# Kernel tuning notes

Measured on AMD Instinct MI355X. Metric: run time of the kernel, lower is better.

Reference implementation:

```python
import jax, jax.numpy as jnp
import numpy as np

BATCH, NODES, FEAT, OUT, EIG = 32, 20000, 64, 64, 16

def setup_inputs() -> dict:
    key = jax.random.key(0)
    k1, k2, k3 = jax.random.split(key, 3)
    x = jax.random.normal(k1, (BATCH, NODES, FEAT), dtype=jnp.float32)
    V = jax.random.normal(k2, (NODES, EIG), dtype=jnp.float32)
    # G packs the ParameterList: G[j, i] == self.G[j*num_features + i]
    # (full EIG x EIG matrices; xavier_uniform_ overwrites the diag init)
    G = jax.random.normal(k3, (OUT, FEAT, EIG, EIG), dtype=jnp.float32) * 0.2
    return {"x": x, "V": V, "G": G}

def reference(x, V, G):
    # original: out[b, n, j] = sum_i (V @ G[j,i] @ V.T @ x[b,:,i]) [n]
    # z[b, i, f] = sum_m V[m, f] * x[b, m, i]        (project onto eigenbasis)
    z = jnp.einsum('mf,bmi->bif', V, x)
    # w[b, j, e] = sum_{i, f} G[j, i, e, f] * z[b, i, f]  (spectral filter mix)
    w = jnp.einsum('jief,bif->bje', G, z)
    # out[b, n, j] = sum_e V[n, e] * w[b, j, e]      (back to node space)
    out = jnp.einsum('ne,bje->bnj', V, w)
    return out
```

## Files before the change

kernel.cpp:

```cpp
#include <hip/hip_runtime.h>

#define BATCH 32
#define NODES 20000
#define FEAT  64
#define OUT   64
#define EIG   16

#define CH1     32
#define S1_NPB  640
#define S1_NPW  160

__global__ void k_zero(float* __restrict__ p, int n) {
    int idx = blockIdx.x * blockDim.x + threadIdx.x;
    if (idx < n) p[idx] = 0.0f;
}

__global__ __launch_bounds__(256)
void k_stage1(const float* __restrict__ x, const float* __restrict__ V,
              float* __restrict__ z) {
    const int c = blockIdx.x;
    const int b = blockIdx.y;
    const int t = threadIdx.x;
    const int lane = t & 63;
    const int wv   = t >> 6;
    const int ms   = lane >> 4;
    const int ig   = lane & 15;

    float4 acc[4][4];
#pragma unroll
    for (int ii = 0; ii < 4; ii++)
#pragma unroll
        for (int q = 0; q < 4; q++) acc[ii][q] = make_float4(0.f,0.f,0.f,0.f);

    const int wb = c * S1_NPB + wv * S1_NPW;
    if (wb < NODES) {
        const float* xp = x + ((size_t)b * NODES + wb + ms) * FEAT + ig * 4;
        const float* vp = V + (size_t)(wb + ms) * EIG;

#pragma unroll 2
        for (int mm = 0; mm < S1_NPW / 4; mm++) {
            const float4 xv = *(const float4*)(xp + (size_t)mm * 4 * FEAT);
            const float4 v0 = *(const float4*)(vp + (size_t)mm * 4 * EIG);
            const float4 v1 = *(const float4*)(vp + (size_t)mm * 4 * EIG + 4);
            const float4 v2 = *(const float4*)(vp + (size_t)mm * 4 * EIG + 8);
            const float4 v3 = *(const float4*)(vp + (size_t)mm * 4 * EIG + 12);
            acc[0][0].x += xv.x*v0.x; acc[0][0].y += xv.x*v0.y; acc[0][0].z += xv.x*v0.z; acc[0][0].w += xv.x*v0.w;
            acc[0][1].x += xv.x*v1.x; acc[0][1].y += xv.x*v1.y; acc[0][1].z += xv.x*v1.z; acc[0][1].w += xv.x*v1.w;
            acc[0][2].x += xv.x*v2.x; acc[0][2].y += xv.x*v2.y; acc[0][2].z += xv.x*v2.z; acc[0][2].w += xv.x*v2.w;
            acc[0][3].x += xv.x*v3.x; acc[0][3].y += xv.x*v3.y; acc[0][3].z += xv.x*v3.z; acc[0][3].w += xv.x*v3.w;
            acc[1][0].x += xv.y*v0.x; acc[1][0].y += xv.y*v0.y; acc[1][0].z += xv.y*v0.z; acc[1][0].w += xv.y*v0.w;
            acc[1][1].x += xv.y*v1.x; acc[1][1].y += xv.y*v1.y; acc[1][1].z += xv.y*v1.z; acc[1][1].w += xv.y*v1.w;
            acc[1][2].x += xv.y*v2.x; acc[1][2].y += xv.y*v2.y; acc[1][2].z += xv.y*v2.z; acc[1][2].w += xv.y*v2.w;
            acc[1][3].x += xv.y*v3.x; acc[1][3].y += xv.y*v3.y; acc[1][3].z += xv.y*v3.z; acc[1][3].w += xv.y*v3.w;
            acc[2][0].x += xv.z*v0.x; acc[2][0].y += xv.z*v0.y; acc[2][0].z += xv.z*v0.z; acc[2][0].w += xv.z*v0.w;
            acc[2][1].x += xv.z*v1.x; acc[2][1].y += xv.z*v1.y; acc[2][1].z += xv.z*v1.z; acc[2][1].w += xv.z*v1.w;
            acc[2][2].x += xv.z*v2.x; acc[2][2].y += xv.z*v2.y; acc[2][2].z += xv.z*v2.z; acc[2][2].w += xv.z*v2.w;
            acc[2][3].x += xv.z*v3.x; acc[2][3].y += xv.z*v3.y; acc[2][3].z += xv.z*v3.z; acc[2][3].w += xv.z*v3.w;
            acc[3][0].x += xv.w*v0.x; acc[3][0].y += xv.w*v0.y; acc[3][0].z += xv.w*v0.z; acc[3][0].w += xv.w*v0.w;
            acc[3][1].x += xv.w*v1.x; acc[3][1].y += xv.w*v1.y; acc[3][1].z += xv.w*v1.z; acc[3][1].w += xv.w*v1.w;
            acc[3][2].x += xv.w*v2.x; acc[3][2].y += xv.w*v2.y; acc[3][2].z += xv.w*v2.z; acc[3][2].w += xv.w*v2.w;
            acc[3][3].x += xv.w*v3.x; acc[3][3].y += xv.w*v3.y; acc[3][3].z += xv.w*v3.z; acc[3][3].w += xv.w*v3.w;
        }
    }

#pragma unroll
    for (int ii = 0; ii < 4; ii++)
#pragma unroll
        for (int q = 0; q < 4; q++) {
            acc[ii][q].x += __shfl_xor(acc[ii][q].x, 16); acc[ii][q].x += __shfl_xor(acc[ii][q].x, 32);
            acc[ii][q].y += __shfl_xor(acc[ii][q].y, 16); acc[ii][q].y += __shfl_xor(acc[ii][q].y, 32);
            acc[ii][q].z += __shfl_xor(acc[ii][q].z, 16); acc[ii][q].z += __shfl_xor(acc[ii][q].z, 32);
            acc[ii][q].w += __shfl_xor(acc[ii][q].w, 16); acc[ii][q].w += __shfl_xor(acc[ii][q].w, 32);
        }

    __shared__ float4 zred[4][16][17];
    if (ms == 0) {
#pragma unroll
        for (int ii = 0; ii < 4; ii++)
#pragma unroll
            for (int q = 0; q < 4; q++) zred[wv][ig][ii * 4 + q] = acc[ii][q];
    }
    __syncthreads();

    const int i = t >> 2, q = t & 3;
    const float4 s0 = zred[0][i >> 2][(i & 3) * 4 + q];
    const float4 s1 = zred[1][i >> 2][(i & 3) * 4 + q];
    const float4 s2 = zred[2][i >> 2][(i & 3) * 4 + q];
    const float4 s3 = zred[3][i >> 2][(i & 3) * 4 + q];
    float* zp = z + (size_t)b * (FEAT * EIG) + (size_t)i * EIG + q * 4;
    atomicAdd(zp + 0, s0.x + s1.x + s2.x + s3.x);
    atomicAdd(zp + 1, s0.y + s1.y + s2.y + s3.y);
    atomicAdd(zp + 2, s0.z + s1.z + s2.z + s3.z);
    atomicAdd(zp + 3, s0.w + s1.w + s2.w + s3.w);
}

__global__ void k_stage2(const float* __restrict__ G, const float* __restrict__ z,
                         float* __restrict__ w) {
    const int j = blockIdx.x;
    const int t = threadIdx.x;
    const int e  = t & 15;
    const int bh = t >> 4;

    __shared__ float zs[32][128];
    const float* Gj = G + (size_t)j * FEAT * EIG * EIG;
    float acc0 = 0.f, acc1 = 0.f;

    for (int i0 = 0; i0 < FEAT; i0 += 8) {
        if (i0) __syncthreads();
#pragma unroll
        for (int r = 0; r < 4; r++) {
            const int g = t + 256 * r;
            const int bb = g >> 5, rem = g & 31;
            ((float4*)&zs[bb][0])[rem] =
                ((const float4*)z)[(size_t)bb * 256 + i0 * 4 + rem];
        }
        __syncthreads();

#pragma unroll 2
        for (int it = 0; it < 8; it++) {
            const int i = i0 + it;
            const float4* gp = (const float4*)(Gj + ((size_t)i * EIG + e) * EIG);
            const float4 g0 = gp[0], g1 = gp[1], g2 = gp[2], g3 = gp[3];
            const float4* zA = (const float4*)&zs[bh][it * 16];
            const float4* zB = (const float4*)&zs[bh + 16][it * 16];
            const float4 a0 = zA[0], a1 = zA[1], a2 = zA[2], a3 = zA[3];
            const float4 b0 = zB[0], b1 = zB[1], b2 = zB[2], b3 = zB[3];
            acc0 += g0.x*a0.x + g0.y*a0.y + g0.z*a0.z + g0.w*a0.w
                  + g1.x*a1.x + g1.y*a1.y + g1.z*a1.z + g1.w*a1.w
                  + g2.x*a2.x + g2.y*a2.y + g2.z*a2.z + g2.w*a2.w
                  + g3.x*a3.x + g3.y*a3.y + g3.z*a3.z + g3.w*a3.w;
            acc1 += g0.x*b0.x + g0.y*b0.y + g0.z*b0.z + g0.w*b0.w
                  + g1.x*b1.x + g1.y*b1.y + g1.z*b1.z + g1.w*b1.w
                  + g2.x*b2.x + g2.y*b2.y + g2.z*b2.z + g2.w*b2.w
                  + g3.x*b3.x + g3.y*b3.y + g3.z*b3.z + g3.w*b3.w;
        }
    }

    w[((size_t)bh * OUT + j) * EIG + e]        = acc0;
    w[((size_t)(bh+16) * OUT + j) * EIG + e]   = acc1;
}

#define DOT16(u) (v0.x*W[u][0].x + v0.y*W[u][0].y + v0.z*W[u][0].z + v0.w*W[u][0].w \
                + v1.x*W[u][1].x + v1.y*W[u][1].y + v1.z*W[u][1].z + v1.w*W[u][1].w \
                + v2.x*W[u][2].x + v2.y*W[u][2].y + v2.z*W[u][2].z + v2.w*W[u][2].w \
                + v3.x*W[u][3].x + v3.y*W[u][3].y + v3.z*W[u][3].z + v3.w*W[u][3].w)

#define CH3 64

__global__ __launch_bounds__(128)
void k_stage3(const float* __restrict__ V, const float* __restrict__ w,
              float* __restrict__ out) {
    const int c = blockIdx.x;
    const int b = blockIdx.y;
    const int t = threadIdx.x;
    const int jg = t & 15;
    const int ns = t >> 4;

    const float* wp = w + ((size_t)b * OUT + 4 * jg) * EIG;
    float4 W[4][4];
#pragma unroll
    for (int u = 0; u < 4; u++)
#pragma unroll
        for (int vr = 0; vr < 4; vr++)
            W[u][vr] = *(const float4*)(wp + u * EIG + vr * 4);

    const int nb = c * 320 + ns;
    float* ob = out + (size_t)b * NODES * OUT + 4 * jg;

#pragma unroll 2
    for (int it = 0; it < 40; it++) {
        const int n = nb + it * 8;
        if (n < NODES) {
            const float* vp = V + (size_t)n * EIG;
            const float4 v0 = *(const float4*)(vp);
            const float4 v1 = *(const float4*)(vp + 4);
            const float4 v2 = *(const float4*)(vp + 8);
            const float4 v3 = *(const float4*)(vp + 12);
            float4 o;
            o.x = DOT16(0);
            o.y = DOT16(1);
            o.z = DOT16(2);
            o.w = DOT16(3);
            *(float4*)(ob + (size_t)n * OUT) = o;
        }
    }
}

extern "C" void kernel_launch(void* const* d_in, const int* in_sizes, int n_in,
                              void* d_out, int out_size, void* d_ws, size_t ws_size,
                              hipStream_t stream) {
    const float* x = (const float*)d_in[0];
    const float* V = (const float*)d_in[1];
    const float* G = (const float*)d_in[2];
    float* out = (float*)d_out;

    float* z = (float*)d_ws;
    float* w = z + (size_t)BATCH * FEAT * EIG;

    const int zn = BATCH * FEAT * EIG;
    k_zero<<<(zn + 255) / 256, 256, 0, stream>>>(z, zn);

    k_stage1<<<dim3(CH1, BATCH), 256, 0, stream>>>(x, V, z);
    k_stage2<<<OUT, 256, 0, stream>>>(G, z, w);
    k_stage3<<<dim3(CH3, BATCH), 128, 0, stream>>>(V, w, out);
}
```

Before: 353.4 us.

## Double-buffer stage1 via LDS async loads, deterministic partial reduction, split stage2, prefetch stage3

Stage1 now streams x and V tiles into LDS with global_load_lds double buffering and writes per-chunk partial sums instead of atomics. A new reduce kernel sums the partials and zeroes w. Stage2 splits the feature loop across 8 blocks per output and accumulates into w with atomics. Stage3 software-prefetches the next V row and sets an occupancy hint. Together these aim to hide load latency and raise parallelism in the small stages, at the cost of an extra launch and partial-buffer traffic.

New measurement: 323.6 us. 1.09x faster.

```diff
diff --git a/kernel.cpp b/kernel.cpp
--- a/kernel.cpp
+++ b/kernel.cpp
@@ -1,4 +1,5 @@
 #include <hip/hip_runtime.h>
+#include <stdint.h>
 
 #define BATCH 32
 #define NODES 20000
@@ -6,18 +7,27 @@
 #define OUT   64
 #define EIG   16
 
-#define CH1     32
-#define S1_NPB  640
-#define S1_NPW  160
-
-__global__ void k_zero(float* __restrict__ p, int n) {
-    int idx = blockIdx.x * blockDim.x + threadIdx.x;
-    if (idx < n) p[idx] = 0.0f;
-}
+#define CH1      25
+#define S1_NPB   800
+#define S1_TILES 10
+#define S1_TR    80
+
+__device__ __forceinline__ void g2l16(const float* g, float* l) {
+    __builtin_amdgcn_global_load_lds(
+        (const __attribute__((address_space(1))) uint32_t*)(uintptr_t)g,
+        (__attribute__((address_space(3))) uint32_t*)(uintptr_t)l,
+        16, 0, 0);
+}
+
+#define FMA16(ii, xc) \
+    acc[ii][0].x += (xc)*v0.x; acc[ii][0].y += (xc)*v0.y; acc[ii][0].z += (xc)*v0.z; acc[ii][0].w += (xc)*v0.w; \
+    acc[ii][1].x += (xc)*v1.x; acc[ii][1].y += (xc)*v1.y; acc[ii][1].z += (xc)*v1.z; acc[ii][1].w += (xc)*v1.w; \
+    acc[ii][2].x += (xc)*v2.x; acc[ii][2].y += (xc)*v2.y; acc[ii][2].z += (xc)*v2.z; acc[ii][2].w += (xc)*v2.w; \
+    acc[ii][3].x += (xc)*v3.x; acc[ii][3].y += (xc)*v3.y; acc[ii][3].z += (xc)*v3.z; acc[ii][3].w += (xc)*v3.w;
 
 __global__ __launch_bounds__(256)
 void k_stage1(const float* __restrict__ x, const float* __restrict__ V,
-              float* __restrict__ z) {
+              float* __restrict__ zpart) {
     const int c = blockIdx.x;
     const int b = blockIdx.y;
     const int t = threadIdx.x;
@@ -26,41 +36,59 @@
     const int ms   = lane >> 4;
     const int ig   = lane & 15;
 
+    __shared__ __align__(16) float xs[2][S1_TR * FEAT];
+    __shared__ __align__(16) float vs[2][S1_TR * EIG];
+
+    const float* xg = x + ((size_t)b * NODES + (size_t)c * S1_NPB) * FEAT;
+    const float* vg = V + (size_t)c * S1_NPB * EIG;
+
+    auto stage = [&](int tt, int d) {
+#pragma unroll
+        for (int k = 0; k < 5; k++) {
+            const int off = wv * 1280 + k * 256;
+            g2l16(xg + (size_t)tt * S1_TR * FEAT + off + lane * 4, &xs[d][off]);
+        }
+#pragma unroll
+        for (int k = 0; k < 2; k++) {
+            const int callid = wv + k * 4;
+            const int off = (callid > 4 ? 4 : callid) * 256;
+            g2l16(vg + (size_t)tt * S1_TR * EIG + off + lane * 4, &vs[d][off]);
+        }
+    };
+
     float4 acc[4][4];
 #pragma unroll
     for (int ii = 0; ii < 4; ii++)
 #pragma unroll
         for (int q = 0; q < 4; q++) acc[ii][q] = make_float4(0.f,0.f,0.f,0.f);
 
-    const int wb = c * S1_NPB + wv * S1_NPW;
-    if (wb < NODES) {
-        const float* xp = x + ((size_t)b * NODES + wb + ms) * FEAT + ig * 4;
-        const float* vp = V + (size_t)(wb + ms) * EIG;
-
-#pragma unroll 2
-        for (int mm = 0; mm < S1_NPW / 4; mm++) {
-            const float4 xv = *(const float4*)(xp + (size_t)mm * 4 * FEAT);
-            const float4 v0 = *(const float4*)(vp + (size_t)mm * 4 * EIG);
-            const float4 v1 = *(const float4*)(vp + (size_t)mm * 4 * EIG + 4);
-            const float4 v2 = *(const float4*)(vp + (size_t)mm * 4 * EIG + 8);
-            const float4 v3 = *(const float4*)(vp + (size_t)mm * 4 * EIG + 12);
-            acc[0][0].x += xv.x*v0.x; acc[0][0].y += xv.x*v0.y; acc[0][0].z += xv.x*v0.z; acc[0][0].w += xv.x*v0.w;
-            acc[0][1].x += xv.x*v1.x; acc[0][1].y += xv.x*v1.y; acc[0][1].z += xv.x*v1.z; acc[0][1].w += xv.x*v1.w;
-            acc[0][2].x += xv.x*v2.x; acc[0][2].y += xv.x*v2.y; acc[0][2].z += xv.x*v2.z; acc[0][2].w += xv.x*v2.w;
-            acc[0][3].x += xv.x*v3.x; acc[0][3].y += xv.x*v3.y; acc[0][3].z += xv.x*v3.z; acc[0][3].w += xv.x*v3.w;
-            acc[1][0].x += xv.y*v0.x; acc[1][0].y += xv.y*v0.y; acc[1][0].z += xv.y*v0.z; acc[1][0].w += xv.y*v0.w;
-            acc[1][1].x += xv.y*v1.x; acc[1][1].y += xv.y*v1.y; acc[1][1].z += xv.y*v1.z; acc[1][1].w += xv.y*v1.w;
-            acc[1][2].x += xv.y*v2.x; acc[1][2].y += xv.y*v2.y; acc[1][2].z += xv.y*v2.z; acc[1][2].w += xv.y*v2.w;
-            acc[1][3].x += xv.y*v3.x; acc[1][3].y += xv.y*v3.y; acc[1][3].z += xv.y*v3.z; acc[1][3].w += xv.y*v3.w;
-            acc[2][0].x += xv.z*v0.x; acc[2][0].y += xv.z*v0.y; acc[2][0].z += xv.z*v0.z; acc[2][0].w += xv.z*v0.w;
-            acc[2][1].x += xv.z*v1.x; acc[2][1].y += xv.z*v1.y; acc[2][1].z += xv.z*v1.z; acc[2][1].w += xv.z*v1.w;
-            acc[2][2].x += xv.z*v2.x; acc[2][2].y += xv.z*v2.y; acc[2][2].z += xv.z*v2.z; acc[2][2].w += xv.z*v2.w;
-            acc[2][3].x += xv.z*v3.x; acc[2][3].y += xv.z*v3.y; acc[2][3].z += xv.z*v3.z; acc[2][3].w += xv.z*v3.w;
-            acc[3][0].x += xv.w*v0.x; acc[3][0].y += xv.w*v0.y; acc[3][0].z += xv.w*v0.z; acc[3][0].w += xv.w*v0.w;
-            acc[3][1].x += xv.w*v1.x; acc[3][1].y += xv.w*v1.y; acc[3][1].z += xv.w*v1.z; acc[3][1].w += xv.w*v1.w;
-            acc[3][2].x += xv.w*v2.x; acc[3][2].y += xv.w*v2.y; acc[3][2].z += xv.w*v2.z; acc[3][2].w += xv.w*v2.w;
-            acc[3][3].x += xv.w*v3.x; acc[3][3].y += xv.w*v3.y; acc[3][3].z += xv.w*v3.z; acc[3][3].w += xv.w*v3.w;
-        }
+    stage(0, 0);
+
+    for (int tt = 0; tt < S1_TILES; tt++) {
+        const int d = tt & 1;
+        if (tt < S1_TILES - 1) {
+            stage(tt + 1, d ^ 1);
+            asm volatile("s_waitcnt vmcnt(7)" ::: "memory");
+        } else {
+            asm volatile("s_waitcnt vmcnt(0)" ::: "memory");
+        }
+        __builtin_amdgcn_s_barrier();
+        __builtin_amdgcn_sched_barrier(0);
+
+        const float* xt = &xs[d][wv * 20 * FEAT];
+        const float* vt = &vs[d][wv * 20 * EIG];
+#pragma unroll
+        for (int itr = 0; itr < 5; itr++) {
+            const int r = itr * 4 + ms;
+            const float4 xv = *(const float4*)(xt + r * FEAT + ig * 4);
+            const float4 v0 = *(const float4*)(vt + r * EIG);
+            const float4 v1 = *(const float4*)(vt + r * EIG + 4);
+            const float4 v2 = *(const float4*)(vt + r * EIG + 8);
+            const float4 v3 = *(const float4*)(vt + r * EIG + 12);
+            FMA16(0, xv.x); FMA16(1, xv.y); FMA16(2, xv.z); FMA16(3, xv.w);
+        }
+        __builtin_amdgcn_sched_barrier(0);
+        __builtin_amdgcn_s_barrier();
     }
 
 #pragma unroll
@@ -73,71 +101,87 @@
             acc[ii][q].w += __shfl_xor(acc[ii][q].w, 16); acc[ii][q].w += __shfl_xor(acc[ii][q].w, 32);
         }
 
-    __shared__ float4 zred[4][16][17];
+    float4* zred = (float4*)&xs[0][0];
+    __syncthreads();
     if (ms == 0) {
 #pragma unroll
         for (int ii = 0; ii < 4; ii++)
 #pragma unroll
-            for (int q = 0; q < 4; q++) zred[wv][ig][ii * 4 + q] = acc[ii][q];
+            for (int q = 0; q < 4; q++)
+                zred[wv * 256 + ig * 16 + ii * 4 + q] = acc[ii][q];
     }
     __syncthreads();
 
-    const int i = t >> 2, q = t & 3;
-    const float4 s0 = zred[0][i >> 2][(i & 3) * 4 + q];
-    const float4 s1 = zred[1][i >> 2][(i & 3) * 4 + q];
-    const float4 s2 = zred[2][i >> 2][(i & 3) * 4 + q];
-    const float4 s3 = zred[3][i >> 2][(i & 3) * 4 + q];
-    float* zp = z + (size_t)b * (FEAT * EIG) + (size_t)i * EIG + q * 4;
-    atomicAdd(zp + 0, s0.x + s1.x + s2.x + s3.x);
-    atomicAdd(zp + 1, s0.y + s1.y + s2.y + s3.y);
-    atomicAdd(zp + 2, s0.z + s1.z + s2.z + s3.z);
-    atomicAdd(zp + 3, s0.w + s1.w + s2.w + s3.w);
+    float4 s  = zred[t];
+    const float4 s1 = zred[256 + t];
+    const float4 s2 = zred[512 + t];
+    const float4 s3 = zred[768 + t];
+    s.x += s1.x + s2.x + s3.x;
+    s.y += s1.y + s2.y + s3.y;
+    s.z += s1.z + s2.z + s3.z;
+    s.w += s1.w + s2.w + s3.w;
+    *(float4*)(zpart + ((size_t)c * BATCH + b) * (FEAT * EIG) + t * 4) = s;
+}
+
+__global__ void k_reduce(const float* __restrict__ zpart, float* __restrict__ z,
+                         float* __restrict__ w) {
+    const int b = blockIdx.y;
+    const int t = threadIdx.x;
+    if (blockIdx.x == 1) {
+        ((float4*)w)[b * 256 + t] = make_float4(0.f, 0.f, 0.f, 0.f);
+        return;
+    }
+    float4 s = make_float4(0.f, 0.f, 0.f, 0.f);
+#pragma unroll
+    for (int c = 0; c < CH1; c++) {
+        const float4 v = ((const float4*)zpart)[((size_t)c * BATCH + b) * 256 + t];
+        s.x += v.x; s.y += v.y; s.z += v.z; s.w += v.w;
+    }
+    ((float4*)z)[(size_t)b * 256 + t] = s;
 }
 
 __global__ void k_stage2(const float* __restrict__ G, const float* __restrict__ z,
                          float* __restrict__ w) {
-    const int j = blockIdx.x;
+    const int j  = blockIdx.x;
+    const int iq = blockIdx.y;
     const int t = threadIdx.x;
     const int e  = t & 15;
     const int bh = t >> 4;
 
     __shared__ float zs[32][128];
+#pragma unroll
+    for (int r = 0; r < 4; r++) {
+        const int g = t + 256 * r;
+        const int bb = g >> 5, off = g & 31;
+        ((float4*)&zs[bb][0])[off] =
+            ((const float4*)z)[(size_t)bb * 256 + iq * 32 + off];
+    }
+    __syncthreads();
+
     const float* Gj = G + (size_t)j * FEAT * EIG * EIG;
     float acc0 = 0.f, acc1 = 0.f;
 
-    for (int i0 = 0; i0 < FEAT; i0 += 8) {
-        if (i0) __syncthreads();
-#pragma unroll
-        for (int r = 0; r < 4; r++) {
-            const int g = t + 256 * r;
-            const int bb = g >> 5, rem = g & 31;
-            ((float4*)&zs[bb][0])[rem] =
-                ((const float4*)z)[(size_t)bb * 256 + i0 * 4 + rem];
-        }
-        __syncthreads();
-
 #pragma unroll 2
-        for (int it = 0; it < 8; it++) {
-            const int i = i0 + it;
-            const float4* gp = (const float4*)(Gj + ((size_t)i * EIG + e) * EIG);
-            const float4 g0 = gp[0], g1 = gp[1], g2 = gp[2], g3 = gp[3];
-            const float4* zA = (const float4*)&zs[bh][it * 16];
-            const float4* zB = (const float4*)&zs[bh + 16][it * 16];
-            const float4 a0 = zA[0], a1 = zA[1], a2 = zA[2], a3 = zA[3];
-            const float4 b0 = zB[0], b1 = zB[1], b2 = zB[2], b3 = zB[3];
-            acc0 += g0.x*a0.x + g0.y*a0.y + g0.z*a0.z + g0.w*a0.w
-                  + g1.x*a1.x + g1.y*a1.y + g1.z*a1.z + g1.w*a1.w
-                  + g2.x*a2.x + g2.y*a2.y + g2.z*a2.z + g2.w*a2.w
-                  + g3.x*a3.x + g3.y*a3.y + g3.z*a3.z + g3.w*a3.w;
-            acc1 += g0.x*b0.x + g0.y*b0.y + g0.z*b0.z + g0.w*b0.w
-                  + g1.x*b1.x + g1.y*b1.y + g1.z*b1.z + g1.w*b1.w
-                  + g2.x*b2.x + g2.y*b2.y + g2.z*b2.z + g2.w*b2.w
-                  + g3.x*b3.x + g3.y*b3.y + g3.z*b3.z + g3.w*b3.w;
-        }
-    }
-
-    w[((size_t)bh * OUT + j) * EIG + e]        = acc0;
-    w[((size_t)(bh+16) * OUT + j) * EIG + e]   = acc1;
+    for (int it = 0; it < 8; it++) {
+        const int i = iq * 8 + it;
+        const float4* gp = (const float4*)(Gj + ((size_t)i * EIG + e) * EIG);
+        const float4 g0 = gp[0], g1 = gp[1], g2 = gp[2], g3 = gp[3];
+        const float4* zA = (const float4*)&zs[bh][it * 16];
+        const float4* zB = (const float4*)&zs[bh + 16][it * 16];
+        const float4 a0 = zA[0], a1 = zA[1], a2 = zA[2], a3 = zA[3];
+        const float4 b0 = zB[0], b1 = zB[1], b2 = zB[2], b3 = zB[3];
+        acc0 += g0.x*a0.x + g0.y*a0.y + g0.z*a0.z + g0.w*a0.w
+              + g1.x*a1.x + g1.y*a1.y + g1.z*a1.z + g1.w*a1.w
+              + g2.x*a2.x + g2.y*a2.y + g2.z*a2.z + g2.w*a2.w
+              + g3.x*a3.x + g3.y*a3.y + g3.z*a3.z + g3.w*a3.w;
+        acc1 += g0.x*b0.x + g0.y*b0.y + g0.z*b0.z + g0.w*b0.w
+              + g1.x*b1.x + g1.y*b1.y + g1.z*b1.z + g1.w*b1.w
+              + g2.x*b2.x + g2.y*b2.y + g2.z*b2.z + g2.w*b2.w
+              + g3.x*b3.x + g3.y*b3.y + g3.z*b3.z + g3.w*b3.w;
+    }
+
+    atomicAdd(&w[((size_t)bh * OUT + j) * EIG + e], acc0);
+    atomicAdd(&w[((size_t)(bh + 16) * OUT + j) * EIG + e], acc1);
 }
 
 #define DOT16(u) (v0.x*W[u][0].x + v0.y*W[u][0].y + v0.z*W[u][0].z + v0.w*W[u][0].w \
@@ -147,7 +191,7 @@
 
 #define CH3 64
 
-__global__ __launch_bounds__(128)
+__global__ __launch_bounds__(128, 4)
 void k_stage3(const float* __restrict__ V, const float* __restrict__ w,
               float* __restrict__ out) {
     const int c = blockIdx.x;
@@ -167,22 +211,31 @@
     const int nb = c * 320 + ns;
     float* ob = out + (size_t)b * NODES * OUT + 4 * jg;
 
-#pragma unroll 2
+    int n = nb;
+    bool val = (n < NODES);
+    float4 v0 = make_float4(0,0,0,0), v1 = v0, v2 = v0, v3 = v0;
+    if (val) {
+        const float* vp = V + (size_t)n * EIG;
+        v0 = *(const float4*)(vp);      v1 = *(const float4*)(vp + 4);
+        v2 = *(const float4*)(vp + 8);  v3 = *(const float4*)(vp + 12);
+    }
+
     for (int it = 0; it < 40; it++) {
-        const int n = nb + it * 8;
-        if (n < NODES) {
-            const float* vp = V + (size_t)n * EIG;
-            const float4 v0 = *(const float4*)(vp);
-            const float4 v1 = *(const float4*)(vp + 4);
-            const float4 v2 = *(const float4*)(vp + 8);
-            const float4 v3 = *(const float4*)(vp + 12);
+        const int n2 = nb + (it + 1) * 8;
+        const bool val2 = (it < 39) && (n2 < NODES);
+        float4 u0 = make_float4(0,0,0,0), u1 = u0, u2 = u0, u3 = u0;
+        if (val2) {
+            const float* vp = V + (size_t)n2 * EIG;
+            u0 = *(const float4*)(vp);      u1 = *(const float4*)(vp + 4);
+            u2 = *(const float4*)(vp + 8);  u3 = *(const float4*)(vp + 12);
+        }
+        if (val) {
             float4 o;
-            o.x = DOT16(0);
-            o.y = DOT16(1);
-            o.z = DOT16(2);
-            o.w = DOT16(3);
+            o.x = DOT16(0); o.y = DOT16(1); o.z = DOT16(2); o.w = DOT16(3);
             *(float4*)(ob + (size_t)n * OUT) = o;
         }
+        v0 = u0; v1 = u1; v2 = u2; v3 = u3;
+        n = n2; val = val2;
     }
 }
 
@@ -194,13 +247,12 @@
     const float* G = (const float*)d_in[2];
     float* out = (float*)d_out;
 
-    float* z = (float*)d_ws;
-    float* w = z + (size_t)BATCH * FEAT * EIG;
-
-    const int zn = BATCH * FEAT * EIG;
-    k_zero<<<(zn + 255) / 256, 256, 0, stream>>>(z, zn);
-
-    k_stage1<<<dim3(CH1, BATCH), 256, 0, stream>>>(x, V, z);
-    k_stage2<<<OUT, 256, 0, stream>>>(G, z, w);
+    float* z     = (float*)d_ws;
+    float* w     = z + (size_t)BATCH * FEAT * EIG;
+    float* zpart = w + (size_t)BATCH * OUT * EIG;
+
+    k_stage1<<<dim3(CH1, BATCH), 256, 0, stream>>>(x, V, zpart);
+    k_reduce<<<dim3(2, BATCH), 256, 0, stream>>>(zpart, z, w);
+    k_stage2<<<dim3(OUT, 8), 256, 0, stream>>>(G, z, w);
     k_stage3<<<dim3(CH3, BATCH), 128, 0, stream>>>(V, w, out);
 }
```
